# Performance work log

Hardware: AMD Instinct MI355X
Metric: run time of the kernel (lower is better)

## Reference

```python
import jax, jax.numpy as jnp
import numpy as np

LN_EPS = 1e-5

def _layernorm(x, g, b):
    mu = jnp.mean(x, axis=-1, keepdims=True)
    var = jnp.var(x, axis=-1, keepdims=True)
    return (x - mu) * jax.lax.rsqrt(var + LN_EPS) * g + b

def setup_inputs() -> dict:
    key = jax.random.key(0)
    ks = jax.random.split(key, 16)
    B, N, dim, dim_out, H = 4, 8192, 128, 256, 4
    hd = dim_out // H
    s = 0.02
    inp = {
        "xyz": jax.random.normal(ks[0], (B, N, 3), jnp.float32),
        "features": jax.random.normal(ks[1], (B, N, dim), jnp.float32),
        "Wq": s * jax.random.normal(ks[2], (dim, dim_out), jnp.float32),
        "bq": jnp.zeros((dim_out,), jnp.float32),
        "Wk": s * jax.random.normal(ks[3], (dim, dim_out), jnp.float32),
        "bk": jnp.zeros((dim_out,), jnp.float32),
        "Wv": s * jax.random.normal(ks[4], (dim, dim_out), jnp.float32),
        "bv": jnp.zeros((dim_out,), jnp.float32),
        "Wp1": s * jax.random.normal(ks[5], (3, hd), jnp.float32),
        "bp1": jnp.zeros((hd,), jnp.float32),
        "Wp2": s * jax.random.normal(ks[6], (hd, hd), jnp.float32),
        "bp2": jnp.zeros((hd,), jnp.float32),
        "Wf1": s * jax.random.normal(ks[7], (dim_out, dim_out), jnp.float32),
        "bf1": jnp.zeros((dim_out,), jnp.float32),
        "Wf2": s * jax.random.normal(ks[8], (dim_out, dim_out), jnp.float32),
        "bf2": jnp.zeros((dim_out,), jnp.float32),
        "g1": jnp.ones((dim,), jnp.float32),
        "b1": jnp.zeros((dim,), jnp.float32),
        "g2": jnp.ones((dim_out,), jnp.float32),
        "b2": jnp.zeros((dim_out,), jnp.float32),
    }
    return inp

def reference(xyz, features, Wq, bq, Wk, bk, Wv, bv, Wp1, bp1, Wp2, bp2,
              Wf1, bf1, Wf2, bf2, g1, b1, g2, b2):
    B, N, _ = xyz.shape
    K = 16
    H = 4
    dim_out = Wq.shape[1]
    hd = dim_out // H

    # KNN via squared pairwise distances (same ordering as torch.cdist)
    sqn = jnp.sum(xyz * xyz, axis=-1)                       # (B,N)
    d2 = sqn[:, :, None] + sqn[:, None, :] - 2.0 * jnp.einsum('bnd,bmd->bnm', xyz, xyz)
    _, knn_idx = jax.lax.top_k(-d2, K)                      # (B,N,K) smallest dists

    bidx = jnp.arange(B)[:, None, None]
    neighbor_xyz = xyz[bidx, knn_idx]                       # (B,N,K,3)
    relative_pos = neighbor_xyz - xyz[:, :, None, :]        # (B,N,K,3)

    # positional encoding MLP: 3 -> hd -> hd
    pos = jax.nn.relu(relative_pos @ Wp1 + bp1) @ Wp2 + bp2 # (B,N,K,hd)

    q = (features @ Wq + bq).reshape(B, N, H, hd)           # (B,N,H,hd)
    nbr_feat = features[bidx, knn_idx]                      # (B,N,K,dim)
    k = (nbr_feat @ Wk + bk).reshape(B, N, K, H, hd)
    v = (nbr_feat @ Wv + bv).reshape(B, N, K, H, hd)

    pos_b = pos[:, :, :, None, :]                           # (B,N,K,1,hd)
    attn = jnp.sum(q[:, :, None, :, :] * (k + pos_b), axis=-1) / jnp.sqrt(jnp.float32(hd))  # (B,N,K,H)
    attn = jax.nn.softmax(attn, axis=2)                     # softmax over neighbors

    out = jnp.sum(attn[..., None] * (v + pos_b), axis=2)    # (B,N,H,hd)
    out = out.reshape(B, N, dim_out)

    fc = jax.nn.relu(out @ Wf1 + bf1) @ Wf2 + bf2
    out = _layernorm(fc, g2, b2) + (_layernorm(features, g1, b1) @ Wq + bq)

    attn_out = jnp.transpose(attn, (0, 3, 1, 2))            # (B,H,N,K) as torch
    return out, attn_out
```

## Files before the change

### kernel.cpp

```cpp
#include <hip/hip_runtime.h>
#include <hip/hip_bf16.h>
#include <math.h>

typedef __hip_bfloat16 bf16;
typedef __attribute__((ext_vector_type(8))) short short8v;
typedef __attribute__((ext_vector_type(4))) float f32x4;

#define NBATCH 4
#define NPTS   8192
#define TOTPTS 32768
#define DIM    128
#define DOUT   256
#define KNN    16

__device__ __forceinline__ float b2f(bf16 x) { return __bfloat162float(x); }
__device__ __forceinline__ bf16 f2b(float x) { return __float2bfloat16(x); }

__device__ __forceinline__ float rsum32(float v) {
#pragma unroll
  for (int o = 16; o; o >>= 1) v += __shfl_down(v, o, 32);
  return v;
}

__global__ __launch_bounds__(256) void pack_kernel(const float* __restrict__ xyz,
                                                   float4* __restrict__ xyzw) {
  const int p = blockIdx.x * 256 + threadIdx.x;
  const float x = xyz[3 * p], y = xyz[3 * p + 1], z = xyz[3 * p + 2];
  xyzw[p] = make_float4(x, y, z, x * x + y * y + z * z);
}

template <int S>
__device__ __forceinline__ void ins16(float d2, int g, int lane, int seg,
                                      float& bd, int& bi, float& tmax) {
  unsigned long long mask = __ballot(d2 < tmax);
  while (mask) {
    const int l = __builtin_ctzll(mask);
    mask &= mask - 1;
    const float dl = __int_as_float(
        __builtin_amdgcn_readlane(__float_as_int(d2), l));
    if (dl < tmax) {
      const int il = g + l;
      const bool keep = bd <= dl;
      const float pd = __shfl_up(bd, 1, 16);
      const int   pi = __shfl_up(bi, 1, 16);
      const bool fromPrev = ((lane & 15) > 0) && (pd > dl);
      const float nbd = keep ? bd : (fromPrev ? pd : dl);
      const int   nbi = keep ? bi : (fromPrev ? pi : il);
      bd = (seg == S) ? nbd : bd;
      bi = (seg == S) ? nbi : bi;
      tmax = __int_as_float(
          __builtin_amdgcn_readlane(__float_as_int(bd), S * 16 + 15));
    }
  }
}

__global__ __launch_bounds__(256) void knn_wave_kernel(
    const float4* __restrict__ xyzw, unsigned short* __restrict__ knn_out) {
  const int wid  = threadIdx.x >> 6;
  const int lane = threadIdx.x & 63;
  const int seg  = lane >> 4;
  const int q0 = (blockIdx.x * 4 + wid) * 4;
  const int b = q0 >> 13;
  const float4* cb = xyzw + (size_t)b * NPTS;

  const float4 mA = xyzw[q0 + 0];
  const float4 mB = xyzw[q0 + 1];
  const float4 mC = xyzw[q0 + 2];
  const float4 mD = xyzw[q0 + 3];

  float bd = INFINITY;
  int   bi = 0x7fff;
  float tA = INFINITY, tB = INFINITY, tC = INFINITY, tD = INFINITY;

  for (int g = 0; g < NPTS; g += 64) {
    const float4 t = cb[g + lane];
    const float dA = mA.w + t.w - 2.f * (mA.x * t.x + mA.y * t.y + mA.z * t.z);
    const float dB = mB.w + t.w - 2.f * (mB.x * t.x + mB.y * t.y + mB.z * t.z);
    const float dC = mC.w + t.w - 2.f * (mC.x * t.x + mC.y * t.y + mC.z * t.z);
    const float dD = mD.w + t.w - 2.f * (mD.x * t.x + mD.y * t.y + mD.z * t.z);
    ins16<0>(dA, g, lane, seg, bd, bi, tA);
    ins16<1>(dB, g, lane, seg, bd, bi, tB);
    ins16<2>(dC, g, lane, seg, bd, bi, tC);
    ins16<3>(dD, g, lane, seg, bd, bi, tD);
  }
  knn_out[(size_t)q0 * KNN + lane] = (unsigned short)bi;
}

__global__ __launch_bounds__(256) void wprep_qkv_kernel(
    const float* __restrict__ Wq, const float* __restrict__ Wk,
    const float* __restrict__ Wv, const float* __restrict__ Wp2,
    bf16* __restrict__ Wqh, bf16* __restrict__ Wql,
    bf16* __restrict__ Wkh, bf16* __restrict__ Wkl,
    bf16* __restrict__ Wvh, bf16* __restrict__ Wvl,
    bf16* __restrict__ W2h, bf16* __restrict__ W2l) {
  const int t = blockIdx.x * 256 + threadIdx.x;
  if (t < 12288) {
    const int m = t >> 12;
    const int rem = t & 4095;
    const int c = rem >> 4, k8 = (rem & 15) * 8;
    const float* src = (m == 0) ? Wq : (m == 1) ? Wk : Wv;
    bf16* dh = (m == 0) ? Wqh : (m == 1) ? Wkh : Wvh;
    bf16* dl = (m == 0) ? Wql : (m == 1) ? Wkl : Wvl;
#pragma unroll
    for (int j = 0; j < 8; j++) {
      const float x = src[(k8 + j) * 256 + c];
      const bf16 hi = f2b(x);
      dh[c * 128 + k8 + j] = hi;
      dl[c * 128 + k8 + j] = f2b(x - b2f(hi));
    }
  } else {
    const int rem = t - 12288;
    const int c = rem >> 3, k8 = (rem & 7) * 8;
#pragma unroll
    for (int j = 0; j < 8; j++) {
      const float x = Wp2[(k8 + j) * 64 + c];
      const bf16 hi = f2b(x);
      W2h[c * 64 + k8 + j] = hi;
      W2l[c * 64 + k8 + j] = f2b(x - b2f(hi));
    }
  }
}

__global__ __launch_bounds__(256) void pos_kernel(
    const float4* __restrict__ xyzw, const unsigned short* __restrict__ knn_in,
    const float* __restrict__ Wp1, const float* __restrict__ bp1,
    const bf16* __restrict__ W2h, const bf16* __restrict__ W2l,
    const float* __restrict__ bp2,
    bf16* __restrict__ posG) {
  const int wid = threadIdx.x >> 6, lane = threadIdx.x & 63;
  const int p = blockIdx.x * 4 + wid;
  const int b = p >> 13, n = p & (NPTS - 1);
  const float4* cb = xyzw + (size_t)b * NPTS;
  const float4 me = cb[n];

  float rx = 0.f, ry = 0.f, rz = 0.f;
  if (lane < 16) {
    const int idx = knn_in[(size_t)p * KNN + lane];
    const float4 t = cb[idx];
    rx = t.x - me.x; ry = t.y - me.y; rz = t.z - me.z;
  }
  const int g = lane >> 4, lr = lane & 15;
  const float r0 = __shfl(rx, lr, 64);
  const float r1 = __shfl(ry, lr, 64);
  const float r2 = __shfl(rz, lr, 64);

  union { short8v v; bf16 e[8]; } ah[2], al[2];
#pragma unroll
  for (int s = 0; s < 2; s++) {
    const int j0 = s * 32 + g * 8;
#pragma unroll
    for (int i = 0; i < 8; i++) {
      const int j = j0 + i;
      const float h = fmaxf(bp1[j] + r0 * Wp1[j] + r1 * Wp1[64 + j]
                                   + r2 * Wp1[128 + j], 0.f);
      const bf16 hh = f2b(h);
      ah[s].e[i] = hh;
      al[s].e[i] = f2b(h - b2f(hh));
    }
  }

  f32x4 acc[4];
#pragma unroll
  for (int t = 0; t < 4; t++) acc[t] = (f32x4){0.f, 0.f, 0.f, 0.f};
#pragma unroll
  for (int s = 0; s < 2; s++) {
    const int k0 = s * 32 + g * 8;
#pragma unroll
    for (int t = 0; t < 4; t++) {
      const int c = 16 * t + lr;
      const short8v bh = *(const short8v*)&W2h[c * 64 + k0];
      const short8v bl = *(const short8v*)&W2l[c * 64 + k0];
      acc[t] = __builtin_amdgcn_mfma_f32_16x16x32_bf16(ah[s].v, bh, acc[t], 0, 0, 0);
      acc[t] = __builtin_amdgcn_mfma_f32_16x16x32_bf16(ah[s].v, bl, acc[t], 0, 0, 0);
      acc[t] = __builtin_amdgcn_mfma_f32_16x16x32_bf16(al[s].v, bh, acc[t], 0, 0, 0);
    }
  }

#pragma unroll
  for (int t = 0; t < 4; t++) {
    const int c = 16 * t + lr;
    const float bb = bp2[c];
#pragma unroll
    for (int e = 0; e < 4; e++) {
      const int row = 4 * g + e;
      posG[((size_t)p * KNN + row) * 64 + c] = f2b(acc[t][e] + bb);
    }
  }
}

#define PR  16
#define PCP 136
__global__ __launch_bounds__(256) void proj_kernel(
    const float* __restrict__ feat,
    const bf16* __restrict__ Wqh, const bf16* __restrict__ Wql,
    const bf16* __restrict__ Wkh, const bf16* __restrict__ Wkl,
    const bf16* __restrict__ Wvh, const bf16* __restrict__ Wvl,
    const float* __restrict__ bq, const float* __restrict__ bk,
    const float* __restrict__ bv,
    const float* __restrict__ g1, const float* __restrict__ b1,
    bf16* __restrict__ Q, bf16* __restrict__ Kf, bf16* __restrict__ Vf,
    float* __restrict__ skip) {
  __shared__ float fS[PR][DIM];
  __shared__ bf16 fh[PR][PCP], fl[PR][PCP];
  __shared__ bf16 lh[PR][PCP], ll[PR][PCP];
  const int tid  = threadIdx.x;
  const size_t r0 = (size_t)blockIdx.x * PR;

  {
    const float4* src = (const float4*)(feat + r0 * DIM);
    float4* dst = (float4*)&fS[0][0];
#pragma unroll
    for (int i = 0; i < 2; i++) dst[tid + i * 256] = src[tid + i * 256];
  }
  __syncthreads();

  {
    const int r = tid >> 4, j = tid & 15;
    float v[8];
    float s = 0.f;
#pragma unroll
    for (int i = 0; i < 8; i++) { v[i] = fS[r][j * 8 + i]; s += v[i]; }
#pragma unroll
    for (int o = 8; o; o >>= 1) s += __shfl_down(s, o, 16);
    const float mu = __shfl(s, 0, 16) * (1.f / 128.f);
    float ss = 0.f;
#pragma unroll
    for (int i = 0; i < 8; i++) { const float d = v[i] - mu; ss += d * d; }
#pragma unroll
    for (int o = 8; o; o >>= 1) ss += __shfl_down(ss, o, 16);
    const float rsd = rsqrtf(__shfl(ss, 0, 16) * (1.f / 128.f) + 1e-5f);
#pragma unroll
    for (int i = 0; i < 8; i++) {
      const int c = j * 8 + i;
      const bf16 hv = f2b(v[i]);
      fh[r][c] = hv;
      fl[r][c] = f2b(v[i] - b2f(hv));
      const float lnv = (v[i] - mu) * rsd * g1[c] + b1[c];
      const bf16 lhv = f2b(lnv);
      lh[r][c] = lhv;
      ll[r][c] = f2b(lnv - b2f(lhv));
    }
  }
  __syncthreads();

  const int w    = tid >> 6;
  const int lane = tid & 63;
  const int g    = lane >> 4, lr = lane & 15;
  const int cw   = w * 64;
  f32x4 qa[4], ka[4], va[4], sa[4];
#pragma unroll
  for (int t = 0; t < 4; t++) {
    qa[t] = (f32x4){0.f, 0.f, 0.f, 0.f};
    ka[t] = qa[t]; va[t] = qa[t]; sa[t] = qa[t];
  }
#pragma unroll
  for (int s = 0; s < 4; s++) {
    const int k0 = s * 32 + g * 8;
    const short8v ah = *(const short8v*)&fh[lr][k0];
    const short8v al = *(const short8v*)&fl[lr][k0];
    const short8v nh = *(const short8v*)&lh[lr][k0];
    const short8v nl = *(const short8v*)&ll[lr][k0];
#pragma unroll
    for (int t = 0; t < 4; t++) {
      const int c = cw + 16 * t + lr;
      const short8v wqh = *(const short8v*)&Wqh[c * 128 + k0];
      const short8v wql = *(const short8v*)&Wql[c * 128 + k0];
      const short8v wkh = *(const short8v*)&Wkh[c * 128 + k0];
      const short8v wkl = *(const short8v*)&Wkl[c * 128 + k0];
      const short8v wvh = *(const short8v*)&Wvh[c * 128 + k0];
      const short8v wvl = *(const short8v*)&Wvl[c * 128 + k0];
      qa[t] = __builtin_amdgcn_mfma_f32_16x16x32_bf16(ah, wqh, qa[t], 0, 0, 0);
      qa[t] = __builtin_amdgcn_mfma_f32_16x16x32_bf16(ah, wql, qa[t], 0, 0, 0);
      qa[t] = __builtin_amdgcn_mfma_f32_16x16x32_bf16(al, wqh, qa[t], 0, 0, 0);
      ka[t] = __builtin_amdgcn_mfma_f32_16x16x32_bf16(ah, wkh, ka[t], 0, 0, 0);
      ka[t] = __builtin_amdgcn_mfma_f32_16x16x32_bf16(ah, wkl, ka[t], 0, 0, 0);
      ka[t] = __builtin_amdgcn_mfma_f32_16x16x32_bf16(al, wkh, ka[t], 0, 0, 0);
      va[t] = __builtin_amdgcn_mfma_f32_16x16x32_bf16(ah, wvh, va[t], 0, 0, 0);
      va[t] = __builtin_amdgcn_mfma_f32_16x16x32_bf16(ah, wvl, va[t], 0, 0, 0);
      va[t] = __builtin_amdgcn_mfma_f32_16x16x32_bf16(al, wvh, va[t], 0, 0, 0);
      sa[t] = __builtin_amdgcn_mfma_f32_16x16x32_bf16(nh, wqh, sa[t], 0, 0, 0);
      sa[t] = __builtin_amdgcn_mfma_f32_16x16x32_bf16(nh, wql, sa[t], 0, 0, 0);
      sa[t] = __builtin_amdgcn_mfma_f32_16x16x32_bf16(nl, wqh, sa[t], 0, 0, 0);
    }
  }

#pragma unroll
  for (int t = 0; t < 4; t++) {
    const int c = cw + 16 * t + lr;
    const float bqv = bq[c], bkv = bk[c], bvv = bv[c];
#pragma unroll
    for (int e = 0; e < 4; e++) {
      const size_t o = (r0 + 4 * g + e) * DOUT + c;
      Q[o]    = f2b(qa[t][e] + bqv);
      Kf[o]   = f2b(ka[t][e] + bkv);
      Vf[o]   = f2b(va[t][e] + bvv);
      skip[o] = sa[t][e] + bqv;
    }
  }
}

__global__ __launch_bounds__(256) void attn_kernel(
    const unsigned short* __restrict__ knn_in,
    bf16* __restrict__ QOA, const bf16* __restrict__ Kf, const bf16* __restrict__ Vf,
    const bf16* __restrict__ posG,
    float* __restrict__ AOUT) {
  __shared__ int nidxS[16];
  const int tid  = threadIdx.x;
  const int w    = tid >> 6;
  const int lane = tid & 63;
  const int p = blockIdx.x;
  const int b = p >> 13, n = p & (NPTS - 1);

  if (tid < 16) nidxS[tid] = knn_in[(size_t)p * KNN + tid];
  const float qreg = b2f(QOA[(size_t)p * DOUT + tid]);
  __syncthreads();

  float kreg[16], vreg[16], posr[16];
  const size_t rowbase = (size_t)b * NPTS;
  const bf16* pg = posG + (size_t)p * KNN * 64 + lane;
#pragma unroll
  for (int k = 0; k < 16; k++) {
    const size_t row = (rowbase + (size_t)nidxS[k]) * DOUT + tid;
    kreg[k] = b2f(Kf[row]);
    vreg[k] = b2f(Vf[row]);
    posr[k] = b2f(pg[k * 64]);
  }

  float lg[16];
#pragma unroll
  for (int k = 0; k < 16; k++) lg[k] = qreg * (kreg[k] + posr[k]);
#pragma unroll
  for (int o = 32; o; o >>= 1) {
#pragma unroll
    for (int k = 0; k < 16; k++) lg[k] += __shfl_xor(lg[k], o, 64);
  }
  float m = -INFINITY;
#pragma unroll
  for (int k = 0; k < 16; k++) { lg[k] *= 0.125f; m = fmaxf(m, lg[k]); }
  float sum = 0.f;
#pragma unroll
  for (int k = 0; k < 16; k++) { lg[k] = expf(lg[k] - m); sum += lg[k]; }
  const float inv = 1.f / sum;
#pragma unroll
  for (int k = 0; k < 16; k++) lg[k] *= inv;
  float av = 0.f;
#pragma unroll
  for (int k = 0; k < 16; k++) if (lane == k) av = lg[k];
  if (lane < 16)
    AOUT[(((size_t)b * 4 + w) * NPTS + n) * KNN + lane] = av;
  float o = 0.f;
#pragma unroll
  for (int k = 0; k < 16; k++) o += lg[k] * (vreg[k] + posr[k]);
  QOA[(size_t)p * DOUT + tid] = f2b(o);
}

__global__ __launch_bounds__(256) void wprep_kernel(
    const float* __restrict__ Wf1, const float* __restrict__ Wf2,
    bf16* __restrict__ Wt1, bf16* __restrict__ Wt2) {
  const int t = blockIdx.x * 256 + threadIdx.x;
  const float* src = (t & 8192) ? Wf2 : Wf1;
  bf16*        dst = (t & 8192) ? Wt2 : Wt1;
  const int rem = t & 8191;
  const int c = rem >> 5, k8 = (rem & 31) * 8;
#pragma unroll
  for (int j = 0; j < 8; j++)
    dst[c * 256 + k8 + j] = f2b(src[(k8 + j) * 256 + c]);
}

#define FRB 16
#define FCP 264
__global__ __launch_bounds__(256) void ffn_kernel(
    const bf16* __restrict__ OA,
    const bf16* __restrict__ Wt1, const float* __restrict__ bf1,
    const bf16* __restrict__ Wt2, const float* __restrict__ bf2,
    const float* __restrict__ g2, const float* __restrict__ b2p,
    float* __restrict__ out) {
  __shared__ float zs[FRB][FCP];
  __shared__ float mu16[FRB], rs16[FRB];
  bf16* base = (bf16*)&zs[0][0];
  const int ysoff = FRB * FCP;
  const int tid  = threadIdx.x;
  const int w    = tid >> 6;
  const int lane = tid & 63;
  const int g    = lane >> 4, lr = lane & 15;
  const int cw   = w * 64;
  const size_t r0 = (size_t)blockIdx.x * FRB;

  {
    const short8v* src = (const short8v*)(OA + r0 * DOUT);
#pragma unroll
    for (int i = 0; i < 2; i++) {
      const int ch = tid + i * 256;
      const int row = ch >> 5, c8 = (ch & 31) * 8;
      *(short8v*)&base[row * FCP + c8] = src[ch];
    }
  }
  __syncthreads();

  f32x4 a0 = {0.f, 0.f, 0.f, 0.f}, a1 = a0, a2 = a0, a3 = a0;

#define GEMM8(OFF, WT)                                                         \
  _Pragma("unroll")                                                            \
  for (int s = 0; s < 8; s++) {                                                \
    const int k0 = s * 32 + g * 8;                                             \
    const short8v av = *(const short8v*)&base[(OFF) + lr * FCP + k0];          \
    a0 = __builtin_amdgcn_mfma_f32_16x16x32_bf16(                              \
        av, *(const short8v*)&(WT)[(cw +  0 + lr) * 256 + k0], a0, 0, 0, 0);   \
    a1 = __builtin_amdgcn_mfma_f32_16x16x32_bf16(                              \
        av, *(const short8v*)&(WT)[(cw + 16 + lr) * 256 + k0], a1, 0, 0, 0);   \
    a2 = __builtin_amdgcn_mfma_f32_16x16x32_bf16(                              \
        av, *(const short8v*)&(WT)[(cw + 32 + lr) * 256 + k0], a2, 0, 0, 0);   \
    a3 = __builtin_amdgcn_mfma_f32_16x16x32_bf16(                              \
        av, *(const short8v*)&(WT)[(cw + 48 + lr) * 256 + k0], a3, 0, 0, 0);   \
  }

  GEMM8(0, Wt1)

#define STORE_Y(ACC, T)                                                        \
  {                                                                            \
    const int c = cw + 16 * (T) + lr;                                          \
    const float bb = bf1[c];                                                   \
    _Pragma("unroll")                                                          \
    for (int e = 0; e < 4; e++)                                                \
      base[ysoff + (4 * g + e) * FCP + c] = f2b(fmaxf(ACC[e] + bb, 0.f));      \
  }
  STORE_Y(a0, 0) STORE_Y(a1, 1) STORE_Y(a2, 2) STORE_Y(a3, 3)
  __syncthreads();

  a0 = (f32x4){0.f, 0.f, 0.f, 0.f}; a1 = a0; a2 = a0; a3 = a0;
  GEMM8(ysoff, Wt2)
  __syncthreads();

#define STORE_Z(ACC, T)                                                        \
  {                                                                            \
    const int c = cw + 16 * (T) + lr;                                          \
    const float bb = bf2[c];                                                   \
    _Pragma("unroll")                                                          \
    for (int e = 0; e < 4; e++) zs[4 * g + e][c] = ACC[e] + bb;                \
  }
  STORE_Z(a0, 0) STORE_Z(a1, 1) STORE_Z(a2, 2) STORE_Z(a3, 3)
  __syncthreads();

  const int r = tid >> 4, j = tid & 15;
  float s = 0.f;
#pragma unroll
  for (int k2 = 0; k2 < 16; k2++) s += zs[r][j + 16 * k2];
#pragma unroll
  for (int o = 8; o; o >>= 1) s += __shfl_down(s, o, 16);
  if (!j) mu16[r] = s * (1.f / 256.f);
  __syncthreads();
  const float mu = mu16[r];
  float ss = 0.f;
#pragma unroll
  for (int k2 = 0; k2 < 16; k2++) { const float dd = zs[r][j + 16 * k2] - mu; ss += dd * dd; }
#pragma unroll
  for (int o = 8; o; o >>= 1) ss += __shfl_down(ss, o, 16);
  if (!j) rs16[r] = rsqrtf(ss * (1.f / 256.f) + 1e-5f);
  __syncthreads();

  const float gv = g2[tid], bbv = b2p[tid];
#pragma unroll
  for (int rr = 0; rr < FRB; rr++) {
    const size_t o = (r0 + rr) * DOUT + tid;
    const float sk = out[o];
    out[o] = (zs[rr][tid] - mu16[rr]) * rs16[rr] * gv + bbv + sk;
  }
}

extern "C" void kernel_launch(void* const* d_in, const int* in_sizes, int n_in,
                              void* d_out, int out_size, void* d_ws, size_t ws_size,
                              hipStream_t stream) {
  const float* xyz  = (const float*)d_in[0];
  const float* feat = (const float*)d_in[1];
  const float* Wq   = (const float*)d_in[2];
  const float* bq   = (const float*)d_in[3];
  const float* Wk   = (const float*)d_in[4];
  const float* bk   = (const float*)d_in[5];
  const float* Wv   = (const float*)d_in[6];
  const float* bv   = (const float*)d_in[7];
  const float* Wp1  = (const float*)d_in[8];
  const float* bp1  = (const float*)d_in[9];
  const float* Wp2  = (const float*)d_in[10];
  const float* bp2  = (const float*)d_in[11];
  const float* Wf1  = (const float*)d_in[12];
  const float* bf1  = (const float*)d_in[13];
  const float* Wf2  = (const float*)d_in[14];
  const float* bf2  = (const float*)d_in[15];
  const float* g1   = (const float*)d_in[16];
  const float* b1   = (const float*)d_in[17];
  const float* g2   = (const float*)d_in[18];
  const float* b2   = (const float*)d_in[19];

  float* out  = (float*)d_out;
  float* aout = out + (size_t)TOTPTS * DOUT;

  unsigned short* knn  = (unsigned short*)d_ws;
  float4*         xyzw = (float4*)aout;
  bf16* QOA  = (bf16*)((char*)d_ws + (size_t)(1 << 20));
  bf16* Kf   = QOA + (size_t)TOTPTS * DOUT;
  bf16* Vf   = Kf  + (size_t)TOTPTS * DOUT;
  bf16* posG = (bf16*)((char*)d_ws + (size_t)(49 << 20));
  bf16* Wt1  = Kf;
  bf16* Wt2  = Kf + 65536;
  bf16* Wqh  = (bf16*)((char*)aout + (512 << 10));
  bf16* Wql  = Wqh + 32768;
  bf16* Wkh  = Wql + 32768;
  bf16* Wkl  = Wkh + 32768;
  bf16* Wvh  = Wkl + 32768;
  bf16* Wvl  = Wvh + 32768;
  bf16* W2h  = Wvl + 32768;
  bf16* W2l  = W2h + 4096;

  pack_kernel<<<TOTPTS / 256, 256, 0, stream>>>(xyz, xyzw);
  wprep_qkv_kernel<<<50, 256, 0, stream>>>(Wq, Wk, Wv, Wp2,
                                           Wqh, Wql, Wkh, Wkl, Wvh, Wvl,
                                           W2h, W2l);
  knn_wave_kernel<<<TOTPTS / 16, 256, 0, stream>>>(xyzw, knn);
  pos_kernel<<<TOTPTS / 4, 256, 0, stream>>>(xyzw, knn, Wp1, bp1, W2h, W2l, bp2,
                                             posG);
  proj_kernel<<<TOTPTS / PR, 256, 0, stream>>>(feat, Wqh, Wql, Wkh, Wkl, Wvh, Wvl,
                                               bq, bk, bv, g1, b1,
                                               QOA, Kf, Vf, out);
  attn_kernel<<<TOTPTS, 256, 0, stream>>>(knn, QOA, Kf, Vf, posG, aout);
  wprep_kernel<<<64, 256, 0, stream>>>(Wf1, Wf2, Wt1, Wt2);
  ffn_kernel<<<TOTPTS / FRB, 256, 0, stream>>>(QOA, Wt1, bf1, Wt2, bf2, g2, b2, out);
}
```

Measured before the change: 674.3 us.

## Fuse positional-encoding MLP into attention kernel via shared memory

```diff
diff --git a/kernel.cpp b/kernel.cpp
--- a/kernel.cpp
+++ b/kernel.cpp
@@ -15,12 +15,6 @@
 
 __device__ __forceinline__ float b2f(bf16 x) { return __bfloat162float(x); }
 __device__ __forceinline__ bf16 f2b(float x) { return __float2bfloat16(x); }
-
-__device__ __forceinline__ float rsum32(float v) {
-#pragma unroll
-  for (int o = 16; o; o >>= 1) v += __shfl_down(v, o, 32);
-  return v;
-}
 
 __global__ __launch_bounds__(256) void pack_kernel(const float* __restrict__ xyz,
                                                    float4* __restrict__ xyzw) {
@@ -121,73 +115,6 @@
   }
 }
 
-__global__ __launch_bounds__(256) void pos_kernel(
-    const float4* __restrict__ xyzw, const unsigned short* __restrict__ knn_in,
-    const float* __restrict__ Wp1, const float* __restrict__ bp1,
-    const bf16* __restrict__ W2h, const bf16* __restrict__ W2l,
-    const float* __restrict__ bp2,
-    bf16* __restrict__ posG) {
-  const int wid = threadIdx.x >> 6, lane = threadIdx.x & 63;
-  const int p = blockIdx.x * 4 + wid;
-  const int b = p >> 13, n = p & (NPTS - 1);
-  const float4* cb = xyzw + (size_t)b * NPTS;
-  const float4 me = cb[n];
-
-  float rx = 0.f, ry = 0.f, rz = 0.f;
-  if (lane < 16) {
-    const int idx = knn_in[(size_t)p * KNN + lane];
-    const float4 t = cb[idx];
-    rx = t.x - me.x; ry = t.y - me.y; rz = t.z - me.z;
-  }
-  const int g = lane >> 4, lr = lane & 15;
-  const float r0 = __shfl(rx, lr, 64);
-  const float r1 = __shfl(ry, lr, 64);
-  const float r2 = __shfl(rz, lr, 64);
-
-  union { short8v v; bf16 e[8]; } ah[2], al[2];
-#pragma unroll
-  for (int s = 0; s < 2; s++) {
-    const int j0 = s * 32 + g * 8;
-#pragma unroll
-    for (int i = 0; i < 8; i++) {
-      const int j = j0 + i;
-      const float h = fmaxf(bp1[j] + r0 * Wp1[j] + r1 * Wp1[64 + j]
-                                   + r2 * Wp1[128 + j], 0.f);
-      const bf16 hh = f2b(h);
-      ah[s].e[i] = hh;
-      al[s].e[i] = f2b(h - b2f(hh));
-    }
-  }
-
-  f32x4 acc[4];
-#pragma unroll
-  for (int t = 0; t < 4; t++) acc[t] = (f32x4){0.f, 0.f, 0.f, 0.f};
-#pragma unroll
-  for (int s = 0; s < 2; s++) {
-    const int k0 = s * 32 + g * 8;
-#pragma unroll
-    for (int t = 0; t < 4; t++) {
-      const int c = 16 * t + lr;
-      const short8v bh = *(const short8v*)&W2h[c * 64 + k0];
-      const short8v bl = *(const short8v*)&W2l[c * 64 + k0];
-      acc[t] = __builtin_amdgcn_mfma_f32_16x16x32_bf16(ah[s].v, bh, acc[t], 0, 0, 0);
-      acc[t] = __builtin_amdgcn_mfma_f32_16x16x32_bf16(ah[s].v, bl, acc[t], 0, 0, 0);
-      acc[t] = __builtin_amdgcn_mfma_f32_16x16x32_bf16(al[s].v, bh, acc[t], 0, 0, 0);
-    }
-  }
-
-#pragma unroll
-  for (int t = 0; t < 4; t++) {
-    const int c = 16 * t + lr;
-    const float bb = bp2[c];
-#pragma unroll
-    for (int e = 0; e < 4; e++) {
-      const int row = 4 * g + e;
-      posG[((size_t)p * KNN + row) * 64 + c] = f2b(acc[t][e] + bb);
-    }
-  }
-}
-
 #define PR  16
 #define PCP 136
 __global__ __launch_bounds__(256) void proj_kernel(
@@ -300,11 +227,14 @@
 }
 
 __global__ __launch_bounds__(256) void attn_kernel(
-    const unsigned short* __restrict__ knn_in,
+    const float4* __restrict__ xyzw, const unsigned short* __restrict__ knn_in,
     bf16* __restrict__ QOA, const bf16* __restrict__ Kf, const bf16* __restrict__ Vf,
-    const bf16* __restrict__ posG,
+    const float* __restrict__ Wp1, const float* __restrict__ bp1,
+    const bf16* __restrict__ W2h, const bf16* __restrict__ W2l,
+    const float* __restrict__ bp2,
     float* __restrict__ AOUT) {
   __shared__ int nidxS[16];
+  __shared__ float posS[16][65];
   const int tid  = threadIdx.x;
   const int w    = tid >> 6;
   const int lane = tid & 63;
@@ -315,20 +245,74 @@
   const float qreg = b2f(QOA[(size_t)p * DOUT + tid]);
   __syncthreads();
 
-  float kreg[16], vreg[16], posr[16];
+  float kreg[16], vreg[16];
   const size_t rowbase = (size_t)b * NPTS;
-  const bf16* pg = posG + (size_t)p * KNN * 64 + lane;
 #pragma unroll
   for (int k = 0; k < 16; k++) {
     const size_t row = (rowbase + (size_t)nidxS[k]) * DOUT + tid;
     kreg[k] = b2f(Kf[row]);
     vreg[k] = b2f(Vf[row]);
-    posr[k] = b2f(pg[k * 64]);
-  }
-
-  float lg[16];
-#pragma unroll
-  for (int k = 0; k < 16; k++) lg[k] = qreg * (kreg[k] + posr[k]);
+  }
+
+  if (w == 0) {
+    const float4* cb = xyzw + rowbase;
+    float rx = 0.f, ry = 0.f, rz = 0.f;
+    if (lane < 16) {
+      const float4 t = cb[nidxS[lane]];
+      const float4 me = cb[n];
+      rx = t.x - me.x; ry = t.y - me.y; rz = t.z - me.z;
+    }
+    const int g = lane >> 4, lr = lane & 15;
+    const float r0 = __shfl(rx, lr, 64);
+    const float r1 = __shfl(ry, lr, 64);
+    const float r2 = __shfl(rz, lr, 64);
+
+    union { short8v v; bf16 e[8]; } ah[2], al[2];
+#pragma unroll
+    for (int s = 0; s < 2; s++) {
+      const int j0 = s * 32 + g * 8;
+#pragma unroll
+      for (int i = 0; i < 8; i++) {
+        const int j = j0 + i;
+        const float h = fmaxf(bp1[j] + r0 * Wp1[j] + r1 * Wp1[64 + j]
+                                     + r2 * Wp1[128 + j], 0.f);
+        const bf16 hh = f2b(h);
+        ah[s].e[i] = hh;
+        al[s].e[i] = f2b(h - b2f(hh));
+      }
+    }
+    f32x4 acc[4];
+#pragma unroll
+    for (int t = 0; t < 4; t++) acc[t] = (f32x4){0.f, 0.f, 0.f, 0.f};
+#pragma unroll
+    for (int s = 0; s < 2; s++) {
+      const int k0 = s * 32 + g * 8;
+#pragma unroll
+      for (int t = 0; t < 4; t++) {
+        const int c = 16 * t + lr;
+        const short8v bh = *(const short8v*)&W2h[c * 64 + k0];
+        const short8v bl = *(const short8v*)&W2l[c * 64 + k0];
+        acc[t] = __builtin_amdgcn_mfma_f32_16x16x32_bf16(ah[s].v, bh, acc[t], 0, 0, 0);
+        acc[t] = __builtin_amdgcn_mfma_f32_16x16x32_bf16(ah[s].v, bl, acc[t], 0, 0, 0);
+        acc[t] = __builtin_amdgcn_mfma_f32_16x16x32_bf16(al[s].v, bh, acc[t], 0, 0, 0);
+      }
+    }
+#pragma unroll
+    for (int t = 0; t < 4; t++) {
+      const int c = 16 * t + lr;
+      const float bb = bp2[c];
+#pragma unroll
+      for (int e = 0; e < 4; e++) posS[4 * g + e][c] = acc[t][e] + bb;
+    }
+  }
+  __syncthreads();
+
+  float posr[16], lg[16];
+#pragma unroll
+  for (int k = 0; k < 16; k++) {
+    posr[k] = posS[k][lane];
+    lg[k] = qreg * (kreg[k] + posr[k]);
+  }
 #pragma unroll
   for (int o = 32; o; o >>= 1) {
 #pragma unroll
@@ -495,14 +479,12 @@
   float* aout = out + (size_t)TOTPTS * DOUT;
 
   unsigned short* knn  = (unsigned short*)d_ws;
-  float4*         xyzw = (float4*)aout;
   bf16* QOA  = (bf16*)((char*)d_ws + (size_t)(1 << 20));
   bf16* Kf   = QOA + (size_t)TOTPTS * DOUT;
   bf16* Vf   = Kf  + (size_t)TOTPTS * DOUT;
-  bf16* posG = (bf16*)((char*)d_ws + (size_t)(49 << 20));
-  bf16* Wt1  = Kf;
-  bf16* Wt2  = Kf + 65536;
-  bf16* Wqh  = (bf16*)((char*)aout + (512 << 10));
+  char* scr  = (char*)d_ws + (size_t)(49 << 20);
+  float4* xyzw = (float4*)scr;
+  bf16* Wqh  = (bf16*)(scr + (512 << 10));
   bf16* Wql  = Wqh + 32768;
   bf16* Wkh  = Wql + 32768;
   bf16* Wkl  = Wkh + 32768;
@@ -510,18 +492,19 @@
   bf16* Wvl  = Wvh + 32768;
   bf16* W2h  = Wvl + 32768;
   bf16* W2l  = W2h + 4096;
+  bf16* Wt1  = Kf;
+  bf16* Wt2  = Kf + 65536;
 
   pack_kernel<<<TOTPTS / 256, 256, 0, stream>>>(xyz, xyzw);
   wprep_qkv_kernel<<<50, 256, 0, stream>>>(Wq, Wk, Wv, Wp2,
                                            Wqh, Wql, Wkh, Wkl, Wvh, Wvl,
                                            W2h, W2l);
   knn_wave_kernel<<<TOTPTS / 16, 256, 0, stream>>>(xyzw, knn);
-  pos_kernel<<<TOTPTS / 4, 256, 0, stream>>>(xyzw, knn, Wp1, bp1, W2h, W2l, bp2,
-                                             posG);
   proj_kernel<<<TOTPTS / PR, 256, 0, stream>>>(feat, Wqh, Wql, Wkh, Wkl, Wvh, Wvl,
                                                bq, bk, bv, g1, b1,
                                                QOA, Kf, Vf, out);
-  attn_kernel<<<TOTPTS, 256, 0, stream>>>(knn, QOA, Kf, Vf, posG, aout);
+  attn_kernel<<<TOTPTS, 256, 0, stream>>>(xyzw, knn, QOA, Kf, Vf,
+                                          Wp1, bp1, W2h, W2l, bp2, aout);
   wprep_kernel<<<64, 256, 0, stream>>>(Wf1, Wf2, Wt1, Wt2);
   ffn_kernel<<<TOTPTS / FRB, 256, 0, stream>>>(QOA, Wt1, bf1, Wt2, bf2, g2, b2, out);
 }
```

After: 655.1 us. 1.03x faster.
